# Kernel optimization log

Hardware: AMD Instinct MI355X
Metric: run time of the kernel (lower is better)

The kernel has to match this reference:

```python
import jax, jax.numpy as jnp
import numpy as np

DIM = 1024
HEADS = 16
HEAD_DIM = DIM // HEADS
THETA = 10000.0


def _freqs_cis(d, n, theta=THETA):
    # complex rotary frequencies, shape (n, d//2)
    pos = jnp.arange(n, dtype=jnp.float32)
    inv = 1.0 / theta ** (jnp.arange(0, d, 2, dtype=jnp.float32) / d)
    ang = jnp.outer(pos, inv)
    return jax.lax.complex(jnp.cos(ang), jnp.sin(ang))


def _to_complex(x):
    # (..., d) -> (..., d//2) complex via adjacent pairs
    xr = x.astype(jnp.float32).reshape(*x.shape[:-1], -1, 2)
    return jax.lax.complex(xr[..., 0], xr[..., 1])


def _to_real(xc):
    # (..., d//2) complex -> (..., d) interleaved real/imag
    return jnp.stack([jnp.real(xc), jnp.imag(xc)], axis=-1).reshape(*xc.shape[:-1], -1)


def setup_inputs() -> dict:
    key = jax.random.key(0)
    k1, k2, k3 = jax.random.split(key, 3)
    b, seq = 2, 2048
    x = jax.random.normal(k1, (b, DIM, seq), dtype=jnp.float32)
    w_qkv = jax.random.normal(k2, (3 * DIM, DIM), dtype=jnp.float32) * (DIM ** -0.5)
    w_out = jax.random.normal(k3, (DIM, DIM), dtype=jnp.float32) * (DIM ** -0.5)
    return {"x": x, "w_qkv": w_qkv, "w_out": w_out}


def reference(x, w_qkv, w_out):
    b, dim, n = x.shape
    h, hd = HEADS, HEAD_DIM
    scale = hd ** -0.5
    xt = jnp.swapaxes(x, -1, -2)                      # (b, t, dim)
    qkv = jnp.einsum('btd,ed->bte', xt, w_qkv)        # (b, t, 3*dim)
    q, k, v = jnp.split(qkv, 3, axis=-1)
    q = q.reshape(b, n, h, hd)
    k = k.reshape(b, n, h, hd)
    v = v.reshape(b, n, h, hd)
    # rotary embedding on q, k
    fc = _freqs_cis(hd, n)[None, :, None, :]          # (1, t, 1, hd//2)
    q = _to_real(_to_complex(q) * fc).astype(x.dtype)
    k = _to_real(_to_complex(k) * fc).astype(x.dtype)
    # naive full attention
    logits = jnp.einsum('bqhd,bkhd->bhqk', q, k) * scale
    probs = jax.nn.softmax(logits, axis=-1)
    out = jnp.einsum('bhqk,bkhd->bqhd', probs, v)     # (b, t, h, hd)
    out = out.reshape(b, n, dim)
    out = jnp.einsum('btd,ed->bte', out, w_out)       # (b, t, dim)
    return jnp.swapaxes(out, -1, -2)                  # (b, dim, t)
```

## Files before the change

### kernel.cpp

```cpp
#include <hip/hip_runtime.h>
#include <hip/hip_bf16.h>
#include <math.h>

#define B 2
#define N 2048
#define D 1024
#define H 16
#define HD 64

typedef __attribute__((ext_vector_type(8))) short short8;
typedef __attribute__((ext_vector_type(4))) float f32x4;
typedef __attribute__((ext_vector_type(16))) float f32x16;
typedef __attribute__((ext_vector_type(4))) unsigned short ush4;
typedef __attribute__((ext_vector_type(4))) unsigned int uint4v;

__device__ __forceinline__ float bf2f(unsigned short u) {
  unsigned int x = ((unsigned int)u) << 16;
  float f;
  __builtin_memcpy(&f, &x, 4);
  return f;
}
__device__ __forceinline__ unsigned short f2bf(float f) {
  unsigned int x;
  __builtin_memcpy(&x, &f, 4);
  x = x + 0x7fffu + ((x >> 16) & 1u);
  return (unsigned short)(x >> 16);
}
__device__ __forceinline__ unsigned int pk2(float lo, float hi) {
  union { __hip_bfloat162 h; unsigned int u; } cv;
  cv.h = __float22bfloat162_rn(make_float2(lo, hi));
  return cv.u;
}
__device__ __forceinline__ short8 mk_frag(unsigned int w0, unsigned int w1,
                                          unsigned int w2, unsigned int w3) {
  union { uint4v u; short8 s; } cv;
  cv.u = (uint4v){w0, w1, w2, w3};
  return cv.s;
}

__device__ __forceinline__ void gload16(const unsigned short* g, unsigned short* l) {
  __builtin_amdgcn_global_load_lds(
      (const __attribute__((address_space(1))) unsigned int*)(const void*)g,
      (__attribute__((address_space(3))) unsigned int*)(void*)l, 16, 0, 0);
}

__global__ void conv_bf16(const float* __restrict__ src, unsigned short* __restrict__ dst, int n4) {
  int i = blockIdx.x * 256 + threadIdx.x;
  if (i >= n4) return;
  float4 v = ((const float4*)src)[i];
  ush4 o;
  o[0] = f2bf(v.x); o[1] = f2bf(v.y); o[2] = f2bf(v.z); o[3] = f2bf(v.w);
  *(ush4*)&dst[i * 4] = o;
}

__global__ __launch_bounds__(256) void transpose_x(const float* __restrict__ x,
                                                   unsigned short* __restrict__ xt) {
  __shared__ float tile[32][33];
  const int tx = threadIdx.x, ty = threadIdx.y;
  const int t0 = blockIdx.x * 32, d0 = blockIdx.y * 32, bb = blockIdx.z;
#pragma unroll
  for (int i = 0; i < 4; ++i) {
    int r = ty * 4 + i;
    tile[r][tx] = x[(size_t)bb * D * N + (size_t)(d0 + r) * N + t0 + tx];
  }
  __syncthreads();
#pragma unroll
  for (int i = 0; i < 4; ++i) {
    int r = ty * 4 + i;
    xt[((size_t)(bb * N) + t0 + r) * D + d0 + tx] = f2bf(tile[tx][r]);
  }
}

__global__ void rope_table(float2* __restrict__ tab) {
  int idx = blockIdx.x * 256 + threadIdx.x;
  int t = idx >> 5, p = idx & 31;
  float inv = powf(10000.f, -(float)p / 32.f);
  float ang = (float)t * inv;
  float s, c;
  sincosf(ang, &s, &c);
  tab[idx] = make_float2(c, s);
}

template <int MODE>
__global__ __launch_bounds__(256) void gemm_bt(const unsigned short* __restrict__ A,
                                               const unsigned short* __restrict__ Bt,
                                               float* __restrict__ outf,
                                               unsigned short* __restrict__ qkbuf,
                                               unsigned short* __restrict__ vtbuf,
                                               const float2* __restrict__ tab) {
  __shared__ unsigned short Asm[128 * 64];
  __shared__ unsigned short Bsm[128 * 64];
  const int tid = threadIdx.x;
  const int lane = tid & 63, wid = tid >> 6;
  const int ln = lane & 15, lh = lane >> 4;
  const int wr = wid >> 1, wc = wid & 1;
  const int m0 = blockIdx.x * 128, n0 = blockIdx.y * 128;

  f32x4 acc[4][4];
#pragma unroll
  for (int i = 0; i < 4; ++i)
#pragma unroll
    for (int j = 0; j < 4; ++j) acc[i][j] = (f32x4){0.f, 0.f, 0.f, 0.f};

  for (int k0 = 0; k0 < 1024; k0 += 64) {
#pragma unroll
    for (int jj = 0; jj < 4; ++jj) {
      int slot = tid + jj * 256;
      int row = slot >> 3, u = slot & 7;
      int usw = (u ^ (row & 7)) * 8;
      gload16(&A[(size_t)(m0 + row) * 1024 + k0 + usw], &Asm[slot * 8]);
    }
#pragma unroll
    for (int jj = 0; jj < 4; ++jj) {
      int slot = tid + jj * 256;
      int row = slot >> 3, u = slot & 7;
      int usw = (u ^ (row & 7)) * 8;
      gload16(&Bt[(size_t)(n0 + row) * 1024 + k0 + usw], &Bsm[slot * 8]);
    }
    __syncthreads();
#pragma unroll
    for (int s = 0; s < 2; ++s) {
      short8 af[4], bfr[4];
#pragma unroll
      for (int i = 0; i < 4; ++i) {
        int row = wr * 64 + i * 16 + ln;
        int u = ((s * 4 + lh) ^ (row & 7)) * 8;
        af[i] = *(const short8*)&Asm[row * 64 + u];
      }
#pragma unroll
      for (int j = 0; j < 4; ++j) {
        int row = wc * 64 + j * 16 + ln;
        int u = ((s * 4 + lh) ^ (row & 7)) * 8;
        bfr[j] = *(const short8*)&Bsm[row * 64 + u];
      }
#pragma unroll
      for (int i = 0; i < 4; ++i)
#pragma unroll
        for (int j = 0; j < 4; ++j)
          acc[i][j] = __builtin_amdgcn_mfma_f32_16x16x32_bf16(af[i], bfr[j], acc[i][j], 0, 0, 0);
    }
    __syncthreads();
  }

  const float qscl = 0.125f * 1.4426950408889634f;
#pragma unroll
  for (int i = 0; i < 4; ++i) {
    int mrow = m0 + wr * 64 + i * 16 + lh * 4;
    int bb = mrow >> 11, t = mrow & 2047;
#pragma unroll
    for (int j = 0; j < 4; ++j) {
      int e = n0 + wc * 64 + j * 16 + ln;
      if (MODE == 1) {
        float* op = outf + (size_t)bb * D * N + (size_t)e * N + t;
        *(f32x4*)op = acc[i][j];
      } else {
        if (e < 2048) {
          float sc = (e < 1024) ? qscl : 1.0f;
          int p0 = (e & 63) >> 1;
          bool odd = e & 1;
#pragma unroll
          for (int jj = 0; jj < 4; ++jj) {
            float a = acc[i][j][jj];
            float pr = __shfl_xor(a, 1, 64);
            float2 cs = tab[(t + jj) * 32 + p0];
            float val = odd ? (pr * cs.y + a * cs.x) : (a * cs.x - pr * cs.y);
            qkbuf[((size_t)(bb * N + t + jj)) * 2048 + e] = f2bf(val * sc);
          }
        } else {
          ush4 v;
#pragma unroll
          for (int jj = 0; jj < 4; ++jj) v[jj] = f2bf(acc[i][j][jj]);
          *(ush4*)&vtbuf[((size_t)bb * 1024 + (e - 2048)) * N + t] = v;
        }
      }
    }
  }
}

__global__ __launch_bounds__(512, 4) void attn_kernel(const unsigned short* __restrict__ qk,
                                                      const unsigned short* __restrict__ vt,
                                                      unsigned short* __restrict__ ob) {
  __shared__ __align__(16) char smem[66048];
  const int tid = threadIdx.x;
  const int lane = tid & 63, wid = tid >> 6;
  const int l31 = lane & 31, hi = lane >> 5;
  const int g = wid >> 2, wl = wid & 3;
  const int tidg = tid & 255;
  const int L = blockIdx.x;
  const int hh = L & 31, qb = L >> 5;
  const int bb = hh >> 4, h = hh & 15;
  const unsigned short* Qg = qk + (size_t)bb * N * 2048 + h * 64;
  const unsigned short* Kg = Qg + 1024;
  const unsigned short* Vg = vt + ((size_t)bb * 1024 + h * 64) * N;

  unsigned short* Ksm[2] = {(unsigned short*)smem + (g * 2 + 0) * 4096,
                            (unsigned short*)smem + (g * 2 + 1) * 4096};
  unsigned short* Vsm[2] = {(unsigned short*)(smem + 32768) + (g * 2 + 0) * 4096,
                            (unsigned short*)(smem + 32768) + (g * 2 + 1) * 4096};

  const int q = qb * 128 + wl * 32 + l31;
  short8 qf[4];
#pragma unroll
  for (int c = 0; c < 4; ++c)
    qf[c] = *(const short8*)&Qg[(size_t)q * 2048 + c * 16 + hi * 8];

  f32x16 oL, oH;
#pragma unroll
  for (int r = 0; r < 16; ++r) { oL[r] = 0.f; oH[r] = 0.f; }
  float lrun = 0.f;

  const int kb0 = g * 1024;
  auto STAGE = [&](int buf, int kb) {
#pragma unroll
    for (int jj = 0; jj < 2; ++jj) {
      int slot = tidg + jj * 256;
      int row = slot >> 3, u = slot & 7;
      int usw = (u ^ (row & 7)) * 8;
      gload16(&Kg[(size_t)(kb + row) * 2048 + usw], &Ksm[buf][slot * 8]);
    }
#pragma unroll
    for (int jj = 0; jj < 2; ++jj) {
      int slot = tidg + jj * 256;
      int row = slot >> 3, u = slot & 7;
      int usw = (u ^ (row & 7)) * 8;
      gload16(&Vg[(size_t)row * N + kb + usw], &Vsm[buf][slot * 8]);
    }
  };

  STAGE(0, kb0);
  __syncthreads();
  int cur = 0;
  for (int t = 0; t < 16; ++t) {
    if (t < 15) STAGE(cur ^ 1, kb0 + (t + 1) * 64);
    f32x16 s0, s1;
#pragma unroll
    for (int r = 0; r < 16; ++r) { s0[r] = 0.f; s1[r] = 0.f; }
    __builtin_amdgcn_s_setprio(1);
#pragma unroll
    for (int c = 0; c < 4; ++c) {
      short8 ka = *(const short8*)&Ksm[cur][l31 * 64 + (((c * 2 + hi) ^ (l31 & 7)) * 8)];
      s0 = __builtin_amdgcn_mfma_f32_32x32x16_bf16(ka, qf[c], s0, 0, 0, 0);
      int r1 = 32 + l31;
      short8 kb2 = *(const short8*)&Ksm[cur][r1 * 64 + (((c * 2 + hi) ^ (r1 & 7)) * 8)];
      s1 = __builtin_amdgcn_mfma_f32_32x32x16_bf16(kb2, qf[c], s1, 0, 0, 0);
    }
    __builtin_amdgcn_s_setprio(0);
    float lsum = 0.f;
#pragma unroll
    for (int r = 0; r < 16; ++r) {
      s0[r] = __builtin_amdgcn_exp2f(s0[r]);
      s1[r] = __builtin_amdgcn_exp2f(s1[r]);
      lsum += s0[r] + s1[r];
    }
    lrun += lsum;
    unsigned int W[16];
#pragma unroll
    for (int i = 0; i < 8; ++i) {
      W[i] = pk2(s0[2 * i], s0[2 * i + 1]);
      W[8 + i] = pk2(s1[2 * i], s1[2 * i + 1]);
    }
    short8 pf[4];
#pragma unroll
    for (int c = 0; c < 4; ++c) {
      unsigned int a0 = W[4 * c + 0], b0 = W[4 * c + 2];
      unsigned int a1 = W[4 * c + 1], b1 = W[4 * c + 3];
      asm volatile("v_permlane32_swap_b32 %0, %1" : "+v"(a0), "+v"(b0));
      asm volatile("v_permlane32_swap_b32 %0, %1" : "+v"(a1), "+v"(b1));
      pf[c] = mk_frag(a0, a1, b0, b1);
    }
    __builtin_amdgcn_s_setprio(1);
#pragma unroll
    for (int c = 0; c < 4; ++c) {
      short8 va = *(const short8*)&Vsm[cur][l31 * 64 + (((c * 2 + hi) ^ (l31 & 7)) * 8)];
      oL = __builtin_amdgcn_mfma_f32_32x32x16_bf16(va, pf[c], oL, 0, 0, 0);
      int rH = 32 + l31;
      short8 vb = *(const short8*)&Vsm[cur][rH * 64 + (((c * 2 + hi) ^ (rH & 7)) * 8)];
      oH = __builtin_amdgcn_mfma_f32_32x32x16_bf16(vb, pf[c], oH, 0, 0, 0);
    }
    __builtin_amdgcn_s_setprio(0);
    __syncthreads();
    cur ^= 1;
  }
  lrun += __shfl_xor(lrun, 32, 64);

  __syncthreads();
  float* cmb = (float*)smem;
  float* lbuf = (float*)(smem + 65536);
  const int ql = wl * 32 + l31;
  if (g) {
#pragma unroll
    for (int r4 = 0; r4 < 4; ++r4) {
      int bo = (ql * 256 + r4 * 32 + hi * 16) ^ ((ql & 7) << 4);
      *(f32x4*)((char*)cmb + bo) =
          (f32x4){oL[r4 * 4], oL[r4 * 4 + 1], oL[r4 * 4 + 2], oL[r4 * 4 + 3]};
      int bo2 = (ql * 256 + 128 + r4 * 32 + hi * 16) ^ ((ql & 7) << 4);
      *(f32x4*)((char*)cmb + bo2) =
          (f32x4){oH[r4 * 4], oH[r4 * 4 + 1], oH[r4 * 4 + 2], oH[r4 * 4 + 3]};
    }
    if (!hi) lbuf[ql] = lrun;
  }
  __syncthreads();
  if (!g) {
#pragma unroll
    for (int r4 = 0; r4 < 4; ++r4) {
      int bo = (ql * 256 + r4 * 32 + hi * 16) ^ ((ql & 7) << 4);
      f32x4 pL = *(const f32x4*)((const char*)cmb + bo);
      int bo2 = (ql * 256 + 128 + r4 * 32 + hi * 16) ^ ((ql & 7) << 4);
      f32x4 pH = *(const f32x4*)((const char*)cmb + bo2);
#pragma unroll
      for (int i = 0; i < 4; ++i) {
        oL[r4 * 4 + i] += pL[i];
        oH[r4 * 4 + i] += pH[i];
      }
    }
    lrun += lbuf[ql];
    float inv = 1.f / lrun;
    unsigned short* obp = ob + ((size_t)(bb * N + q)) * 1024 + h * 64;
#pragma unroll
    for (int r4 = 0; r4 < 4; ++r4) {
      ush4 vL, vH;
#pragma unroll
      for (int i = 0; i < 4; ++i) {
        vL[i] = f2bf(oL[r4 * 4 + i] * inv);
        vH[i] = f2bf(oH[r4 * 4 + i] * inv);
      }
      *(ush4*)&obp[r4 * 8 + hi * 4] = vL;
      *(ush4*)&obp[32 + r4 * 8 + hi * 4] = vH;
    }
  }
}

extern "C" void kernel_launch(void* const* d_in, const int* in_sizes, int n_in,
                              void* d_out, int out_size, void* d_ws, size_t ws_size,
                              hipStream_t stream) {
  const float* x = (const float*)d_in[0];
  const float* w_qkv = (const float*)d_in[1];
  const float* w_out = (const float*)d_in[2];
  float* out = (float*)d_out;
  char* ws = (char*)d_ws;

  unsigned short* wqkv_bf = (unsigned short*)ws;
  unsigned short* wout_bf = (unsigned short*)(ws + 6291456);
  unsigned short* xt      = (unsigned short*)(ws + 8388608);
  unsigned short* qkbuf   = (unsigned short*)(ws + 16777216);
  unsigned short* vtbuf   = (unsigned short*)(ws + 33554432);
  float2* tab             = (float2*)(ws + 41943040);

  conv_bf16<<<3072, 256, 0, stream>>>(w_qkv, wqkv_bf, 3072 * 1024 / 4);
  conv_bf16<<<1024, 256, 0, stream>>>(w_out, wout_bf, 1024 * 1024 / 4);
  rope_table<<<256, 256, 0, stream>>>(tab);
  transpose_x<<<dim3(N / 32, D / 32, B), dim3(32, 8), 0, stream>>>(x, xt);

  gemm_bt<0><<<dim3(32, 24), 256, 0, stream>>>(xt, wqkv_bf, nullptr, qkbuf, vtbuf, tab);
  attn_kernel<<<512, 512, 0, stream>>>(qkbuf, vtbuf, xt );
  gemm_bt<1><<<dim3(32, 8), 256, 0, stream>>>(xt, wout_bf, out, nullptr, nullptr, nullptr);
}
```

Baseline: 140.4 us.

## Merge weight conversion and rope table kernels; move rotary to separate pass

Combines the two weight bf16 conversions and the rope table build into one launch. It also removes the rotary embedding and Q scaling from the QKV GEMM epilogue and applies them in a new vectorized kernel over the bf16 Q/K buffer. This shrinks the GEMM epilogue (no shuffles or table loads) and saves two launches. In exchange it adds a full read and write of the 16 MB QK buffer and one more launch, and rotary is now applied after bf16 rounding, which adds a second rounding step.

New measurement: 133.4 us. 5.0% less time.

```diff
diff --git a/kernel.cpp b/kernel.cpp
--- a/kernel.cpp
+++ b/kernel.cpp
@@ -44,13 +44,27 @@
       (__attribute__((address_space(3))) unsigned int*)(void*)l, 16, 0, 0);
 }
 
-__global__ void conv_bf16(const float* __restrict__ src, unsigned short* __restrict__ dst, int n4) {
-  int i = blockIdx.x * 256 + threadIdx.x;
-  if (i >= n4) return;
-  float4 v = ((const float4*)src)[i];
-  ush4 o;
-  o[0] = f2bf(v.x); o[1] = f2bf(v.y); o[2] = f2bf(v.z); o[3] = f2bf(v.w);
-  *(ush4*)&dst[i * 4] = o;
+__global__ void prep_k(const float* __restrict__ wqkv, unsigned short* __restrict__ wqkv_bf,
+                       const float* __restrict__ wout, unsigned short* __restrict__ wout_bf,
+                       float2* __restrict__ tab) {
+  int blk = blockIdx.x;
+  if (blk < 4096) {
+    const float* src = (blk < 3072) ? wqkv : wout;
+    unsigned short* dst = (blk < 3072) ? wqkv_bf : wout_bf;
+    int i = (blk < 3072 ? blk : blk - 3072) * 256 + threadIdx.x;
+    float4 v = ((const float4*)src)[i];
+    ush4 o;
+    o[0] = f2bf(v.x); o[1] = f2bf(v.y); o[2] = f2bf(v.z); o[3] = f2bf(v.w);
+    *(ush4*)&dst[i * 4] = o;
+  } else {
+    int idx = (blk - 4096) * 256 + threadIdx.x;
+    int t = idx >> 5, p = idx & 31;
+    float inv = powf(10000.f, -(float)p / 32.f);
+    float ang = (float)t * inv;
+    float s, c;
+    sincosf(ang, &s, &c);
+    tab[idx] = make_float2(c, s);
+  }
 }
 
 __global__ __launch_bounds__(256) void transpose_x(const float* __restrict__ x,
@@ -71,23 +85,12 @@
   }
 }
 
-__global__ void rope_table(float2* __restrict__ tab) {
-  int idx = blockIdx.x * 256 + threadIdx.x;
-  int t = idx >> 5, p = idx & 31;
-  float inv = powf(10000.f, -(float)p / 32.f);
-  float ang = (float)t * inv;
-  float s, c;
-  sincosf(ang, &s, &c);
-  tab[idx] = make_float2(c, s);
-}
-
 template <int MODE>
 __global__ __launch_bounds__(256) void gemm_bt(const unsigned short* __restrict__ A,
                                                const unsigned short* __restrict__ Bt,
                                                float* __restrict__ outf,
                                                unsigned short* __restrict__ qkbuf,
-                                               unsigned short* __restrict__ vtbuf,
-                                               const float2* __restrict__ tab) {
+                                               unsigned short* __restrict__ vtbuf) {
   __shared__ unsigned short Asm[128 * 64];
   __shared__ unsigned short Bsm[128 * 64];
   const int tid = threadIdx.x;
@@ -142,7 +145,6 @@
     __syncthreads();
   }
 
-  const float qscl = 0.125f * 1.4426950408889634f;
 #pragma unroll
   for (int i = 0; i < 4; ++i) {
     int mrow = m0 + wr * 64 + i * 16 + lh * 4;
@@ -155,17 +157,9 @@
         *(f32x4*)op = acc[i][j];
       } else {
         if (e < 2048) {
-          float sc = (e < 1024) ? qscl : 1.0f;
-          int p0 = (e & 63) >> 1;
-          bool odd = e & 1;
-#pragma unroll
-          for (int jj = 0; jj < 4; ++jj) {
-            float a = acc[i][j][jj];
-            float pr = __shfl_xor(a, 1, 64);
-            float2 cs = tab[(t + jj) * 32 + p0];
-            float val = odd ? (pr * cs.y + a * cs.x) : (a * cs.x - pr * cs.y);
-            qkbuf[((size_t)(bb * N + t + jj)) * 2048 + e] = f2bf(val * sc);
-          }
+#pragma unroll
+          for (int jj = 0; jj < 4; ++jj)
+            qkbuf[((size_t)(bb * N + t + jj)) * 2048 + e] = f2bf(acc[i][j][jj]);
         } else {
           ush4 v;
 #pragma unroll
@@ -175,6 +169,27 @@
       }
     }
   }
+}
+
+__global__ void rope_kernel(unsigned short* __restrict__ qk, const float2* __restrict__ tab) {
+  int idx = blockIdx.x * 256 + threadIdx.x;
+  int e = (idx & 255) * 8;
+  int t = (idx >> 8) & 2047;
+  int bb = idx >> 19;
+  int p0 = (e & 63) >> 1;
+  const float qscl = 0.125f * 1.4426950408889634f;
+  float sc = (e < 1024) ? qscl : 1.0f;
+  unsigned short* p = qk + ((size_t)(bb * N + t)) * 2048 + e;
+  short8 v = *(short8*)p;
+#pragma unroll
+  for (int q = 0; q < 4; ++q) {
+    float2 cs = tab[t * 32 + p0 + q];
+    float xe = bf2f((unsigned short)v[2 * q]);
+    float xo = bf2f((unsigned short)v[2 * q + 1]);
+    v[2 * q] = (short)f2bf((xe * cs.x - xo * cs.y) * sc);
+    v[2 * q + 1] = (short)f2bf((xe * cs.y + xo * cs.x) * sc);
+  }
+  *(short8*)p = v;
 }
 
 __global__ __launch_bounds__(512, 4) void attn_kernel(const unsigned short* __restrict__ qk,
@@ -346,12 +361,11 @@
   unsigned short* vtbuf   = (unsigned short*)(ws + 33554432);
   float2* tab             = (float2*)(ws + 41943040);
 
-  conv_bf16<<<3072, 256, 0, stream>>>(w_qkv, wqkv_bf, 3072 * 1024 / 4);
-  conv_bf16<<<1024, 256, 0, stream>>>(w_out, wout_bf, 1024 * 1024 / 4);
-  rope_table<<<256, 256, 0, stream>>>(tab);
+  prep_k<<<4352, 256, 0, stream>>>(w_qkv, wqkv_bf, w_out, wout_bf, tab);
   transpose_x<<<dim3(N / 32, D / 32, B), dim3(32, 8), 0, stream>>>(x, xt);
 
-  gemm_bt<0><<<dim3(32, 24), 256, 0, stream>>>(xt, wqkv_bf, nullptr, qkbuf, vtbuf, tab);
+  gemm_bt<0><<<dim3(32, 24), 256, 0, stream>>>(xt, wqkv_bf, nullptr, qkbuf, vtbuf);
+  rope_kernel<<<4096, 256, 0, stream>>>(qkbuf, tab);
   attn_kernel<<<512, 512, 0, stream>>>(qkbuf, vtbuf, xt );
-  gemm_bt<1><<<dim3(32, 8), 256, 0, stream>>>(xt, wout_bf, out, nullptr, nullptr, nullptr);
-}
+  gemm_bt<1><<<dim3(32, 8), 256, 0, stream>>>(xt, wout_bf, out, nullptr, nullptr);
+}
```
